# Kernel optimization log

Measured on AMD Instinct MI355X. Metric: run time of the kernel, lower is better.

## Reference

```python
import jax, jax.numpy as jnp
import numpy as np

SIZE, D, N, E = 50000, 1024, 50000, 100000


def setup_inputs() -> dict:
    key = jax.random.key(0)
    k1, k2 = jax.random.split(key)
    # torchhd.embeddings.Random produces bipolar {-1,+1} MAP hypervectors
    w = jnp.where(jax.random.uniform(k1, (SIZE, D)) < 0.5, -1.0, 1.0).astype(jnp.float32)
    edge_index = jax.random.randint(k2, (2, E), 0, N, dtype=jnp.int32)
    return {"node_ids_weight": w, "edge_index": edge_index, "num_nodes": N}


def reference(node_ids_weight, edge_index, num_nodes):
    # degree_centrality: in-degree via bincount on columns, normalized
    col = edge_index[1]
    degree = jnp.bincount(col, length=num_nodes)
    pr = degree / num_nodes  # float
    pr_argsort = jnp.argsort(pr)  # stable sort, matches torch sort semantics on ties

    # node_id_hvs[pr_argsort] = weight[:num_nodes]  (scatter assign)
    node_id_hvs = jnp.zeros((num_nodes, node_ids_weight.shape[1]),
                            dtype=node_ids_weight.dtype)
    node_id_hvs = node_id_hvs.at[pr_argsort].set(node_ids_weight[:num_nodes])

    # to_undirected: sort endpoints per edge, then unique columns.
    # jit-friendly unique: lexsort edges, mask out duplicates of the previous edge.
    e = jnp.sort(edge_index, axis=0)  # [2, E], row <= col per edge
    order = jnp.lexsort((e[1], e[0]))
    r = e[0][order]
    c = e[1][order]
    keep = jnp.concatenate([
        jnp.array([True]),
        (r[1:] != r[:-1]) | (c[1:] != c[:-1]),
    ])  # [E] True for first occurrence of each unique edge

    # bind = elementwise multiply of gathered hvs; multiset = sum over edges
    hvs = node_id_hvs[r] * node_id_hvs[c]  # [E, D]
    out = jnp.sum(jnp.where(keep[:, None], hvs, 0.0), axis=0)  # [D]
    return out
```

## Files before the change

### kernel.cpp

```cpp
#include <hip/hip_runtime.h>
#include <stdint.h>

#define DCAP   128
#define CHUNK  1024
#define LOG_TAB 19
#define TAB_SIZE (1u << LOG_TAB)
#define TAB_MASK (TAB_SIZE - 1u)
#define KEMPTY 0xFFFFFFFFu

__global__ void k_degree(const int* __restrict__ col, int* __restrict__ degree, int E) {
    int e = blockIdx.x * blockDim.x + threadIdx.x;
    if (e < E) atomicAdd(&degree[col[e]], 1);
}

__global__ void k_chunk_hist(const int* __restrict__ degree, int* __restrict__ hist,
                             int* __restrict__ chunkHist, int N) {
    __shared__ int sh[DCAP];
    int t = threadIdx.x;
    if (t < DCAP) sh[t] = 0;
    __syncthreads();
    int j = blockIdx.x * CHUNK + t;
    if (j < N) {
        int d = degree[j];
        if (d < DCAP) atomicAdd(&sh[d], 1);
        else          atomicAdd(&hist[d], 1);
    }
    __syncthreads();
    if (t < DCAP) chunkHist[blockIdx.x * DCAP + t] = sh[t];
}

__global__ void k_chunk_prefix(int* __restrict__ hist, int* __restrict__ chunkHist,
                               int numChunks) {
    __shared__ int stot[DCAP];
    int d = threadIdx.x;
    int tot = 0;
    for (int c = 0; c < numChunks; ++c) tot += chunkHist[c * DCAP + d];
    stot[d] = tot;
    hist[d] = tot;
    __syncthreads();
    int run = 0;
    for (int d2 = 0; d2 < d; ++d2) run += stot[d2];
    for (int c = 0; c < numChunks; ++c) {
        int tmp = chunkHist[c * DCAP + d];
        chunkHist[c * DCAP + d] = run;
        run += tmp;
    }
}

__global__ void k_pos_small(const int* __restrict__ degree, const int* __restrict__ chunkBase,
                            int* __restrict__ pos, int N) {
    __shared__ int sdeg[CHUNK];
    int t = threadIdx.x;
    int j = blockIdx.x * CHUNK + t;
    int d = (j < N) ? degree[j] : -1;
    sdeg[t] = d;
    __syncthreads();
    if (j < N && d < DCAP) {
        int r = 0;
        for (int t2 = 0; t2 < t; ++t2) r += (sdeg[t2] == d);
        pos[j] = chunkBase[blockIdx.x * DCAP + d] + r;
    }
}

__global__ void k_pos_large(const int* __restrict__ degree, const int* __restrict__ hist,
                            int* __restrict__ pos, int N, int E) {
    int d = DCAP + blockIdx.x * blockDim.x + threadIdx.x;
    if (d > E) return;
    if (hist[d] == 0) return;
    int base = 0;
    for (int d2 = 0; d2 < d; ++d2) base += hist[d2];
    int cnt = 0;
    for (int j = 0; j < N; ++j)
        if (degree[j] == d) pos[j] = base + cnt++;
}

__global__ __launch_bounds__(256) void k_pack(const float* __restrict__ W,
                                              uint32_t* __restrict__ Wbits, long long NW) {
    long long widx = (long long)blockIdx.x * 256 + threadIdx.x;
    if (widx >= NW) return;
    const uint4* src = (const uint4*)(W + widx * 32);
    uint32_t word = 0;
    #pragma unroll
    for (int q = 0; q < 8; ++q) {
        uint4 u = src[q];
        word |= (u.x >> 31) << (4 * q + 0);
        word |= (u.y >> 31) << (4 * q + 1);
        word |= (u.z >> 31) << (4 * q + 2);
        word |= (u.w >> 31) << (4 * q + 3);
    }
    Wbits[widx] = word;
}

__global__ void k_insert(const int* __restrict__ ei, const int* __restrict__ pos,
                         unsigned int* __restrict__ tab, int* __restrict__ uA,
                         int* __restrict__ uB, int* __restrict__ count, int E) {
    int e = blockIdx.x * blockDim.x + threadIdx.x;
    if (e >= E) return;
    int a = ei[e], b = ei[E + e];
    int r = min(a, b), c = max(a, b);
    unsigned int key = ((unsigned int)r << 16) | (unsigned int)c;
    unsigned int h = (key * 2654435761u) >> (32 - LOG_TAB);
    while (true) {
        unsigned int old = atomicCAS(&tab[h], KEMPTY, key);
        if (old == KEMPTY) {
            int idx = atomicAdd(count, 1);
            uA[idx] = pos[r];
            uB[idx] = pos[c];
            return;
        }
        if (old == key) return;
        h = (h + 1) & TAB_MASK;
    }
}

__global__ __launch_bounds__(256) void k_accum_bits(const uint32_t* __restrict__ Wbits,
                                                    const int* __restrict__ uA,
                                                    const int* __restrict__ uB,
                                                    const int* __restrict__ count,
                                                    int* __restrict__ neg, int D) {
    __shared__ int sneg[1024];
    int t = threadIdx.x;
    int w = t & 31;
    int slot = t >> 5;
    int wpr = D / 32;
    for (int i = t; i < D; i += 256) sneg[i] = 0;
    __syncthreads();
    int cnt = *count;
    int cnts[32];
    #pragma unroll
    for (int d = 0; d < 32; ++d) cnts[d] = 0;
    for (int base = blockIdx.x * 8; base < cnt; base += gridDim.x * 8) {
        int e = base + slot;
        if (e < cnt) {
            uint32_t a = Wbits[(size_t)uA[e] * wpr + w];
            uint32_t b = Wbits[(size_t)uB[e] * wpr + w];
            uint32_t x = a ^ b;
            #pragma unroll
            for (int d = 0; d < 32; ++d) cnts[d] += (x >> d) & 1u;
        }
    }
    #pragma unroll
    for (int d = 0; d < 32; ++d) atomicAdd(&sneg[w * 32 + d], cnts[d]);
    __syncthreads();
    for (int i = t; i < D; i += 256)
        if (sneg[i]) atomicAdd(&neg[i], sneg[i]);
}

__global__ void k_finalize(const int* __restrict__ neg, const int* __restrict__ count,
                           float* __restrict__ out, int D) {
    int d = blockIdx.x * blockDim.x + threadIdx.x;
    if (d < D) out[d] = (float)(*count - 2 * neg[d]);
}

static inline size_t align256(size_t x) { return (x + 255) & ~(size_t)255; }

extern "C" void kernel_launch(void* const* d_in, const int* in_sizes, int n_in,
                              void* d_out, int out_size, void* d_ws, size_t ws_size,
                              hipStream_t stream) {
    const float* W  = (const float*)d_in[0];
    const int*   ei = (const int*)d_in[1];
    const int D = out_size;
    const int N = in_sizes[0] / D;
    const int E = in_sizes[1] / 2;
    const int numChunks = (N + CHUNK - 1) / CHUNK;
    const long long ND = (long long)N * D;
    const long long NW = ND / 32;

    char* p = (char*)d_ws;
    int* degree       = (int*)p;          p += align256((size_t)N * 4);
    int* hist         = (int*)p;          p += align256((size_t)(E + 1) * 4);
    int* chunkHist    = (int*)p;          p += align256((size_t)numChunks * DCAP * 4);
    int* pos          = (int*)p;          p += align256((size_t)N * 4);
    unsigned int* tab = (unsigned int*)p; p += (size_t)TAB_SIZE * 4;
    int* uA           = (int*)p;          p += align256((size_t)E * 4);
    int* uB           = (int*)p;          p += align256((size_t)E * 4);
    int* count        = (int*)p;          p += 256;
    int* neg          = (int*)p;          p += align256((size_t)D * 4);
    uint32_t* Wbits   = (uint32_t*)p;     p += align256((size_t)NW * 4);

    hipMemsetAsync(degree, 0, (size_t)N * 4, stream);
    hipMemsetAsync(hist, 0, (size_t)(E + 1) * 4, stream);
    hipMemsetAsync(tab, 0xFF, (size_t)TAB_SIZE * 4, stream);
    hipMemsetAsync(count, 0, 4, stream);
    hipMemsetAsync(neg, 0, (size_t)D * 4, stream);

    k_degree<<<(E + 255) / 256, 256, 0, stream>>>(ei + E, degree, E);
    k_chunk_hist<<<numChunks, CHUNK, 0, stream>>>(degree, hist, chunkHist, N);
    k_chunk_prefix<<<1, DCAP, 0, stream>>>(hist, chunkHist, numChunks);
    k_pos_small<<<numChunks, CHUNK, 0, stream>>>(degree, chunkHist, pos, N);
    int nLarge = E + 1 - DCAP;
    k_pos_large<<<(nLarge + 255) / 256, 256, 0, stream>>>(degree, hist, pos, N, E);
    k_pack<<<(int)((NW + 255) / 256), 256, 0, stream>>>(W, Wbits, NW);
    k_insert<<<(E + 255) / 256, 256, 0, stream>>>(ei, pos, tab, uA, uB, count, E);
    k_accum_bits<<<1024, 256, 0, stream>>>(Wbits, uA, uB, count, neg, D);
    k_finalize<<<(D + 255) / 256, 256, 0, stream>>>(neg, count, (float*)d_out, D);
}
```

Measured before the change: 145.2 us.

## Pack sign bits via wave ballot, fuse finalize into accumulate, merge memsets

Replaces the per-thread strided 32-float sign-packing loop with a coalesced uint4 load per thread and wavefront ballots. Words are stored in a permuted bit order, which the final un-permute mapping corrects. The finalize kernel is folded into the accumulation kernel using a last-block-done counter, and the several zeroing memsets are merged into one contiguous memset. The aim is to make the dominant 200MB read of W coalesced and to cut launch overhead, at the cost of bit-order complexity and an extra atomic counter.

```diff
diff --git a/kernel.cpp b/kernel.cpp
--- a/kernel.cpp
+++ b/kernel.cpp
@@ -74,8 +74,26 @@
         if (degree[j] == d) pos[j] = base + cnt++;
 }
 
-__global__ __launch_bounds__(256) void k_pack(const float* __restrict__ W,
-                                              uint32_t* __restrict__ Wbits, long long NW) {
+__global__ __launch_bounds__(256) void k_pack_ballot(const float* __restrict__ W,
+                                                     uint32_t* __restrict__ Wbits) {
+    long long idx = (long long)blockIdx.x * 256 + threadIdx.x;
+    const uint4 u = ((const uint4*)W)[idx];
+    int lane = threadIdx.x & 63;
+    unsigned long long m0 = __ballot((int)u.x < 0);
+    unsigned long long m1 = __ballot((int)u.y < 0);
+    unsigned long long m2 = __ballot((int)u.z < 0);
+    unsigned long long m3 = __ballot((int)u.w < 0);
+    if (lane < 8) {
+        int k = lane >> 1, half = lane & 1;
+        unsigned long long m = (k == 0) ? m0 : (k == 1) ? m1 : (k == 2) ? m2 : m3;
+        uint32_t w32 = half ? (uint32_t)(m >> 32) : (uint32_t)m;
+        long long gwave = idx >> 6;
+        Wbits[gwave * 8 + lane] = w32;
+    }
+}
+
+__global__ __launch_bounds__(256) void k_pack_linear(const float* __restrict__ W,
+                                                     uint32_t* __restrict__ Wbits, long long NW) {
     long long widx = (long long)blockIdx.x * 256 + threadIdx.x;
     if (widx >= NW) return;
     const uint4* src = (const uint4*)(W + widx * 32);
@@ -117,8 +135,12 @@
                                                     const int* __restrict__ uA,
                                                     const int* __restrict__ uB,
                                                     const int* __restrict__ count,
-                                                    int* __restrict__ neg, int D) {
+                                                    int* __restrict__ neg,
+                                                    int* __restrict__ done,
+                                                    float* __restrict__ out,
+                                                    int D, int permuted) {
     __shared__ int sneg[1024];
+    __shared__ int lastFlag;
     int t = threadIdx.x;
     int w = t & 31;
     int slot = t >> 5;
@@ -144,12 +166,24 @@
     __syncthreads();
     for (int i = t; i < D; i += 256)
         if (sneg[i]) atomicAdd(&neg[i], sneg[i]);
-}
-
-__global__ void k_finalize(const int* __restrict__ neg, const int* __restrict__ count,
-                           float* __restrict__ out, int D) {
-    int d = blockIdx.x * blockDim.x + threadIdx.x;
-    if (d < D) out[d] = (float)(*count - 2 * neg[d]);
+
+    __threadfence();
+    if (t == 0) lastFlag = (atomicAdd(done, 1) == (int)gridDim.x - 1);
+    __syncthreads();
+    if (lastFlag) {
+        for (int d = t; d < D; d += 256) {
+            int ni;
+            if (permuted) {
+                int off = d & 255, q = d >> 8;
+                int k = off & 3, l = off >> 2, half = l >> 5, b = l & 31;
+                ni = (q * 8 + 2 * k + half) * 32 + b;
+            } else {
+                ni = d;
+            }
+            int nv = atomicAdd(&neg[ni], 0);
+            out[d] = (float)(cnt - 2 * nv);
+        }
+    }
 }
 
 static inline size_t align256(size_t x) { return (x + 255) & ~(size_t)255; }
@@ -167,22 +201,22 @@
     const long long NW = ND / 32;
 
     char* p = (char*)d_ws;
+    char* zbase = p;
     int* degree       = (int*)p;          p += align256((size_t)N * 4);
     int* hist         = (int*)p;          p += align256((size_t)(E + 1) * 4);
+    int* count        = (int*)p;          p += 256;
+    int* done         = (int*)p;          p += 256;
+    int* neg          = (int*)p;          p += align256((size_t)D * 4);
+    size_t zbytes = (size_t)(p - zbase);
     int* chunkHist    = (int*)p;          p += align256((size_t)numChunks * DCAP * 4);
     int* pos          = (int*)p;          p += align256((size_t)N * 4);
     unsigned int* tab = (unsigned int*)p; p += (size_t)TAB_SIZE * 4;
     int* uA           = (int*)p;          p += align256((size_t)E * 4);
     int* uB           = (int*)p;          p += align256((size_t)E * 4);
-    int* count        = (int*)p;          p += 256;
-    int* neg          = (int*)p;          p += align256((size_t)D * 4);
     uint32_t* Wbits   = (uint32_t*)p;     p += align256((size_t)NW * 4);
 
-    hipMemsetAsync(degree, 0, (size_t)N * 4, stream);
-    hipMemsetAsync(hist, 0, (size_t)(E + 1) * 4, stream);
+    hipMemsetAsync(zbase, 0, zbytes, stream);
     hipMemsetAsync(tab, 0xFF, (size_t)TAB_SIZE * 4, stream);
-    hipMemsetAsync(count, 0, 4, stream);
-    hipMemsetAsync(neg, 0, (size_t)D * 4, stream);
 
     k_degree<<<(E + 255) / 256, 256, 0, stream>>>(ei + E, degree, E);
     k_chunk_hist<<<numChunks, CHUNK, 0, stream>>>(degree, hist, chunkHist, N);
@@ -190,8 +224,15 @@
     k_pos_small<<<numChunks, CHUNK, 0, stream>>>(degree, chunkHist, pos, N);
     int nLarge = E + 1 - DCAP;
     k_pos_large<<<(nLarge + 255) / 256, 256, 0, stream>>>(degree, hist, pos, N, E);
-    k_pack<<<(int)((NW + 255) / 256), 256, 0, stream>>>(W, Wbits, NW);
+
+    int permuted = (D % 256 == 0) && (ND % 1024 == 0);
+    if (permuted) {
+        k_pack_ballot<<<(int)(ND / 1024), 256, 0, stream>>>(W, Wbits);
+    } else {
+        k_pack_linear<<<(int)((NW + 255) / 256), 256, 0, stream>>>(W, Wbits, NW);
+    }
+
     k_insert<<<(E + 255) / 256, 256, 0, stream>>>(ei, pos, tab, uA, uB, count, E);
-    k_accum_bits<<<1024, 256, 0, stream>>>(Wbits, uA, uB, count, neg, D);
-    k_finalize<<<(D + 255) / 256, 256, 0, stream>>>(neg, count, (float*)d_out, D);
-}
+    k_accum_bits<<<1024, 256, 0, stream>>>(Wbits, uA, uB, count, neg, done,
+                                           (float*)d_out, D, permuted);
+}
```

After: 181.2 us. 24.8% more time.
